# Kernel optimization log

Measured on AMD Instinct MI355X. Metric: run time of the kernel, lower is better.

## Reference

```python
import jax, jax.numpy as jnp
import numpy as np

D_MODEL = 256
D_HEAD = 64
N_HEAD = 8


def setup_inputs() -> dict:
    key = jax.random.key(0)
    ks = jax.random.split(key, 8)
    b, h, w = 32, 64, 64
    dk = D_HEAD * N_HEAD
    s = 1.0 / np.sqrt(D_MODEL)
    x = jax.random.normal(ks[0], (b, D_MODEL, h, w), dtype=jnp.float32)
    query = jax.random.normal(ks[1], (b, D_MODEL), dtype=jnp.float32)
    Wkv = jax.random.uniform(ks[2], (2 * dk, D_MODEL), jnp.float32, -s, s)
    bkv = jax.random.uniform(ks[3], (2 * dk,), jnp.float32, -s, s)
    Wq = jax.random.uniform(ks[4], (dk, D_MODEL), jnp.float32, -s, s)
    bq = jax.random.uniform(ks[5], (dk,), jnp.float32, -s, s)
    sf = 1.0 / np.sqrt(dk)
    Wfc = jax.random.uniform(ks[6], (D_MODEL, dk), jnp.float32, -sf, sf)
    bfc = jax.random.uniform(ks[7], (D_MODEL,), jnp.float32, -sf, sf)
    return {"x": x, "query": query, "Wkv": Wkv, "bkv": bkv, "Wq": Wq, "bq": bq, "Wfc": Wfc, "bfc": bfc}


def reference(x, query, Wkv, bkv, Wq, bq, Wfc, bfc):
    b, c, h, w = x.shape
    t = h * w
    scale = 1.0 / np.sqrt(D_HEAD).astype(np.float32)
    # 1x1 conv == per-pixel linear: (b, 2*n*d, t)
    kv = jnp.einsum('bchw,oc->bohw', x, Wkv).reshape(b, 2 * N_HEAD, D_HEAD, t)
    kv = kv + bkv.reshape(1, 2 * N_HEAD, D_HEAD, 1)
    k, v = kv[:, :N_HEAD], kv[:, N_HEAD:]  # each (b, n, d, t)
    q = (query @ Wq.T + bq).reshape(b, N_HEAD, D_HEAD)
    logits = jnp.einsum('bnd,bndj->bnj', q, k) * scale
    attn = jax.nn.softmax(logits, axis=2)
    out = jnp.einsum('bnj,bndj->bnd', attn, v).reshape(b, N_HEAD * D_HEAD)
    return jax.nn.relu(out @ Wfc.T + bfc)
```

## Files before the change

### kernel.cpp

```cpp
#include <hip/hip_runtime.h>
#include <hip/hip_bf16.h>

#define B_     32
#define C_     256
#define T_     4096
#define NH_    8
#define DH_    64

__global__ __launch_bounds__(256) void k_prep(
    const float* __restrict__ query, const float* __restrict__ Wkv,
    const float* __restrict__ bkv, const float* __restrict__ Wq,
    const float* __restrict__ bq, float* __restrict__ qWt,
    float* __restrict__ qb) {
  const int n = blockIdx.x;
  const int b = blockIdx.y;
  const int t = threadIdx.x;
  __shared__ float qrow_s[C_];
  __shared__ float psum[4 * 64];
  __shared__ float qsh[64];
  __shared__ float pb_s[64];

  qrow_s[t] = query[(size_t)b * C_ + t];
  __syncthreads();

  {
    const int d = t & 63, ch = t >> 6;
    const float* wrow = Wq + (size_t)(n * DH_ + d) * C_ + ch * 64;
    const float* qr = qrow_s + ch * 64;
    float s = 0.f;
    #pragma unroll
    for (int c = 0; c < 64; c += 4) {
      float4 w = *(const float4*)(wrow + c);
      s += w.x * qr[c] + w.y * qr[c + 1] + w.z * qr[c + 2] + w.w * qr[c + 3];
    }
    psum[ch * 64 + d] = s;
  }
  __syncthreads();
  if (t < 64)
    qsh[t] = bq[n * DH_ + t] + psum[t] + psum[64 + t] + psum[128 + t] + psum[192 + t];
  __syncthreads();

  const float scale = 0.125f;
  {
    const float* wk = Wkv + (size_t)(n * DH_) * C_ + t;
    float acc = 0.f;
    #pragma unroll 8
    for (int dd = 0; dd < DH_; ++dd) acc += qsh[dd] * wk[(size_t)dd * C_];
    qWt[((size_t)b * C_ + t) * NH_ + n] = acc * scale;
  }
  if (t < 64) pb_s[t] = qsh[t] * bkv[n * DH_ + t];
  __syncthreads();
  if (t == 0) {
    float s = 0.f;
    #pragma unroll 8
    for (int dd = 0; dd < 64; ++dd) s += pb_s[dd];
    qb[b * NH_ + n] = s * scale;
  }
}

__global__ __launch_bounds__(256) void k_logits(
    const float* __restrict__ x, const float* __restrict__ qWt,
    const float* __restrict__ qbv, float* __restrict__ lgpart) {
  const int half = blockIdx.y;
  const int b = blockIdx.z;
  const int t = threadIdx.x;
  const int j = blockIdx.x * 512 + t * 2;
  __shared__ float qws[128 * NH_];

  {
    const float4 v = *(const float4*)(qWt + (size_t)b * (C_ * NH_) + half * 1024 + t * 4);
    *(float4*)(qws + t * 4) = v;
  }
  __syncthreads();

  const float* xb = x + ((size_t)b * C_ + half * 128) * T_ + j;
  const float* qb = qbv + b * NH_;

  float acc0[NH_], acc1[NH_];
  #pragma unroll
  for (int n = 0; n < NH_; ++n) {
    const float init = half ? 0.f : qb[n];
    acc0[n] = init; acc1[n] = init;
  }

  for (int c0 = 0; c0 < 128; c0 += 8) {
    float2 xv[8];
    #pragma unroll
    for (int cc = 0; cc < 8; ++cc)
      xv[cc] = *(const float2*)(xb + (size_t)(c0 + cc) * T_);
    #pragma unroll
    for (int cc = 0; cc < 8; ++cc) {
      const float4 w0 = *(const float4*)(qws + (c0 + cc) * 8);
      const float4 w1 = *(const float4*)(qws + (c0 + cc) * 8 + 4);
      acc0[0] += w0.x * xv[cc].x; acc1[0] += w0.x * xv[cc].y;
      acc0[1] += w0.y * xv[cc].x; acc1[1] += w0.y * xv[cc].y;
      acc0[2] += w0.z * xv[cc].x; acc1[2] += w0.z * xv[cc].y;
      acc0[3] += w0.w * xv[cc].x; acc1[3] += w0.w * xv[cc].y;
      acc0[4] += w1.x * xv[cc].x; acc1[4] += w1.x * xv[cc].y;
      acc0[5] += w1.y * xv[cc].x; acc1[5] += w1.y * xv[cc].y;
      acc0[6] += w1.z * xv[cc].x; acc1[6] += w1.z * xv[cc].y;
      acc0[7] += w1.w * xv[cc].x; acc1[7] += w1.w * xv[cc].y;
    }
  }

  float* lg = lgpart + (((size_t)half * B_ + b) * NH_) * T_ + j;
  #pragma unroll
  for (int n = 0; n < NH_; ++n) {
    float2 o; o.x = acc0[n]; o.y = acc1[n];
    *(float2*)(lg + (size_t)n * T_) = o;
  }
}

__global__ __launch_bounds__(256) void k_softmax(
    const float* __restrict__ lgpart, float* __restrict__ attn) {
  const size_t row = blockIdx.x;
  const float* p0 = lgpart + row * T_;
  const float* p1 = lgpart + ((size_t)B_ * NH_ + row) * T_;
  float* pa = attn + row * T_;
  const int t = threadIdx.x;
  float4 v[4];
  #pragma unroll
  for (int i = 0; i < 4; ++i) {
    float4 a = *(const float4*)(p0 + t * 4 + i * 1024);
    float4 c = *(const float4*)(p1 + t * 4 + i * 1024);
    v[i].x = a.x + c.x; v[i].y = a.y + c.y; v[i].z = a.z + c.z; v[i].w = a.w + c.w;
  }

  float m = -3.4e38f;
  #pragma unroll
  for (int i = 0; i < 4; ++i)
    m = fmaxf(m, fmaxf(fmaxf(v[i].x, v[i].y), fmaxf(v[i].z, v[i].w)));
  #pragma unroll
  for (int o = 32; o >= 1; o >>= 1) m = fmaxf(m, __shfl_xor(m, o));
  __shared__ float sm[4];
  if ((t & 63) == 0) sm[t >> 6] = m;
  __syncthreads();
  m = fmaxf(fmaxf(sm[0], sm[1]), fmaxf(sm[2], sm[3]));

  float s = 0.f;
  #pragma unroll
  for (int i = 0; i < 4; ++i) {
    v[i].x = expf(v[i].x - m); v[i].y = expf(v[i].y - m);
    v[i].z = expf(v[i].z - m); v[i].w = expf(v[i].w - m);
    s += v[i].x + v[i].y + v[i].z + v[i].w;
  }
  #pragma unroll
  for (int o = 32; o >= 1; o >>= 1) s += __shfl_xor(s, o);
  __shared__ float ss[4];
  if ((t & 63) == 0) ss[t >> 6] = s;
  __syncthreads();
  s = ss[0] + ss[1] + ss[2] + ss[3];
  const float inv = 1.0f / s;

  #pragma unroll
  for (int i = 0; i < 4; ++i) {
    v[i].x *= inv; v[i].y *= inv; v[i].z *= inv; v[i].w *= inv;
    *(float4*)(pa + t * 4 + i * 1024) = v[i];
  }
}

#define BJ_  256
#define BJS_ 32
#define XPITCH_ 33
__global__ __launch_bounds__(256) void k_xattn(
    const float* __restrict__ x, const float* __restrict__ attn,
    float* __restrict__ part) {
  const int jt = blockIdx.x;
  const int b  = blockIdx.y;
  const int j0 = jt * BJ_;
  const int t  = threadIdx.x;
  __shared__ float xs[C_ * XPITCH_];

  const float* xb = x + (size_t)b * C_ * T_;
  const float* ab = attn + (size_t)b * NH_ * T_ + j0;

  float acc[NH_];
  #pragma unroll
  for (int n = 0; n < NH_; ++n) acc[n] = 0.f;

  const int cr = t >> 3;
  const int jc = (t & 7) * 4;

  for (int sIt = 0; sIt < BJ_ / BJS_; ++sIt) {
    const int js = sIt * BJS_;
    __syncthreads();
    #pragma unroll
    for (int p = 0; p < 8; ++p) {
      const int c = cr + p * 32;
      float4 vv = *(const float4*)(xb + (size_t)c * T_ + j0 + js + jc);
      float* dst = &xs[c * XPITCH_ + jc];
      dst[0] = vv.x; dst[1] = vv.y; dst[2] = vv.z; dst[3] = vv.w;
    }
    __syncthreads();
    const float* xr = &xs[t * XPITCH_];
    #pragma unroll 4
    for (int jj = 0; jj < BJS_; ++jj) {
      const float xv = xr[jj];
      const int j = js + jj;
      #pragma unroll
      for (int n = 0; n < NH_; ++n)
        acc[n] += ab[(size_t)n * T_ + j] * xv;
    }
  }

  float* pb = part + ((size_t)b * 16 + jt) * (NH_ * C_);
  #pragma unroll
  for (int n = 0; n < NH_; ++n) pb[n * C_ + t] = acc[n];
}

__global__ __launch_bounds__(512) void k_tail(
    const float* __restrict__ part, const float* __restrict__ Wkv,
    const float* __restrict__ bkv, const float* __restrict__ Wfc,
    const float* __restrict__ bfc, float* __restrict__ out) {
  __shared__ float xa_s[NH_ * C_];
  __shared__ float ov[512];
  const int b = blockIdx.x;
  const int t = threadIdx.x;

  const float* pb = part + (size_t)b * 16 * (NH_ * C_);
  #pragma unroll
  for (int r = 0; r < 4; ++r) {
    const int idx = r * 512 + t;
    float s = 0.f;
    #pragma unroll
    for (int jt = 0; jt < 16; ++jt) s += pb[(size_t)jt * (NH_ * C_) + idx];
    xa_s[idx] = s;
  }
  __syncthreads();

  {
    const int o = t;
    const float* wrow = Wkv + (size_t)(512 + o) * C_;
    const float* xa = &xa_s[(o >> 6) * C_];
    float s = bkv[512 + o];
    #pragma unroll 8
    for (int c = 0; c < C_; c += 4) {
      float4 w = *(const float4*)(wrow + c);
      s += w.x * xa[c] + w.y * xa[c + 1] + w.z * xa[c + 2] + w.w * xa[c + 3];
    }
    ov[o] = s;
  }
  __syncthreads();

  if (t < 256) {
    const int m = t;
    const float* wrow = Wfc + (size_t)m * 512;
    float s = bfc[m];
    #pragma unroll 8
    for (int o = 0; o < 512; o += 4) {
      float4 w = *(const float4*)(wrow + o);
      s += w.x * ov[o] + w.y * ov[o + 1] + w.z * ov[o + 2] + w.w * ov[o + 3];
    }
    out[(size_t)b * 256 + m] = fmaxf(s, 0.f);
  }
}

extern "C" void kernel_launch(void* const* d_in, const int* in_sizes, int n_in,
                              void* d_out, int out_size, void* d_ws, size_t ws_size,
                              hipStream_t stream) {
  const float* x     = (const float*)d_in[0];
  const float* query = (const float*)d_in[1];
  const float* Wkv   = (const float*)d_in[2];
  const float* bkv   = (const float*)d_in[3];
  const float* Wq    = (const float*)d_in[4];
  const float* bq    = (const float*)d_in[5];
  const float* Wfc   = (const float*)d_in[6];
  const float* bfc   = (const float*)d_in[7];
  float* out = (float*)d_out;
  float* ws  = (float*)d_ws;

  float* qWt    = ws;
  float* qb     = ws + 65536;
  float* lgpart = ws + 66048;
  float* attn   = ws + 2163200;
  float* part   = ws + 3211776;

  k_prep   <<<dim3(NH_, B_),   256, 0, stream>>>(query, Wkv, bkv, Wq, bq, qWt, qb);
  k_logits <<<dim3(8, 2, B_),  256, 0, stream>>>(x, qWt, qb, lgpart);
  k_softmax<<<B_ * NH_,        256, 0, stream>>>(lgpart, attn);
  k_xattn  <<<dim3(16, B_),    256, 0, stream>>>(x, attn, part);
  k_tail   <<<B_,              512, 0, stream>>>(part, Wkv, bkv, Wfc, bfc, out);
}
```

Baseline: 277.9 us.

## Fuse logits, softmax and attention-weighted x into one tiled split-softmax kernel

Replaces the separate logits, softmax and x·attn kernels with one kernel that loads each 64-column tile of x into shared memory once. It computes logits, local max and exponentials, and partial weighted sums per tile, then a merge kernel rescales the partials with the tile statistics (a flash-decoding-style split softmax). This removes the second full read of x and the global round trips for logits and attention weights. In exchange it writes larger partials (64 tiles per batch), serialises the per-tile softmax on 8 threads, and uses about 75KB of shared memory per block, which limits occupancy.

```diff
diff --git a/kernel.cpp b/kernel.cpp
--- a/kernel.cpp
+++ b/kernel.cpp
@@ -6,6 +6,9 @@
 #define T_     4096
 #define NH_    8
 #define DH_    64
+#define JT_    64
+#define NT_    (T_ / JT_)
+#define XP_    65
 
 __global__ __launch_bounds__(256) void k_prep(
     const float* __restrict__ query, const float* __restrict__ Wkv,
@@ -58,158 +61,137 @@
   }
 }
 
-__global__ __launch_bounds__(256) void k_logits(
+__global__ __launch_bounds__(256) void k_fused(
     const float* __restrict__ x, const float* __restrict__ qWt,
-    const float* __restrict__ qbv, float* __restrict__ lgpart) {
-  const int half = blockIdx.y;
-  const int b = blockIdx.z;
+    const float* __restrict__ qbv, float* __restrict__ part,
+    float* __restrict__ stats) {
+  const int tile = blockIdx.x;
+  const int b    = blockIdx.y;
+  const int t    = threadIdx.x;
+  const int j0   = tile * JT_;
+
+  __shared__ float xs[C_ * XP_];
+  __shared__ float lsc[4 * 576];
+  float* const ew = lsc + 576;
+
+  const float* xb = x + (size_t)b * C_ * T_ + j0;
+
+  {
+    const int cg = t >> 4;
+    const int jc = (t & 15) * 4;
+    #pragma unroll 4
+    for (int p = 0; p < 16; ++p) {
+      const int c = cg + p * 16;
+      float4 v = *(const float4*)(xb + (size_t)c * T_ + jc);
+      float* d = &xs[c * XP_ + jc];
+      d[0] = v.x; d[1] = v.y; d[2] = v.z; d[3] = v.w;
+    }
+  }
+  __syncthreads();
+
+  {
+    const int j  = t & 63;
+    const int ch = t >> 6;
+    const float* qw = qWt + ((size_t)b * C_ + ch * 64) * NH_;
+    float al[NH_];
+    #pragma unroll
+    for (int n = 0; n < NH_; ++n) al[n] = 0.f;
+    #pragma unroll 4
+    for (int cc = 0; cc < 64; ++cc) {
+      const float xv = xs[(ch * 64 + cc) * XP_ + j];
+      const float* qwc = qw + cc * NH_;
+      #pragma unroll
+      for (int n = 0; n < NH_; ++n) al[n] += qwc[n] * xv;
+    }
+    float* dst = &lsc[ch * 576 + j * 9];
+    #pragma unroll
+    for (int n = 0; n < NH_; ++n) dst[n] = al[n];
+  }
+  __syncthreads();
+
+  {
+    const float* qb = qbv + b * NH_;
+    #pragma unroll
+    for (int r = 0; r < 2; ++r) {
+      const int s = r * 256 + t;
+      const int j = s >> 3, n = s & 7;
+      const int idx = j * 9 + n;
+      const float l = lsc[idx] + lsc[576 + idx] + lsc[1152 + idx] +
+                      lsc[1728 + idx] + qb[n];
+      lsc[idx] = l;
+    }
+  }
+  __syncthreads();
+
+  if (t < NH_) {
+    float m = -3.4e38f;
+    for (int j = 0; j < JT_; ++j) m = fmaxf(m, lsc[j * 9 + t]);
+    float s = 0.f;
+    for (int j = 0; j < JT_; ++j) {
+      const float e = __expf(lsc[j * 9 + t] - m);
+      ew[j * 8 + t] = e;
+      s += e;
+    }
+    float* st = stats + (((size_t)b * NT_ + tile) * NH_ + t) * 2;
+    st[0] = m; st[1] = s;
+  }
+  __syncthreads();
+
+  {
+    float acc[NH_];
+    #pragma unroll
+    for (int n = 0; n < NH_; ++n) acc[n] = 0.f;
+    const float* xr = &xs[t * XP_];
+    #pragma unroll 4
+    for (int j = 0; j < JT_; ++j) {
+      const float xv = xr[j];
+      const float4 e0 = *(const float4*)(ew + j * 8);
+      const float4 e1 = *(const float4*)(ew + j * 8 + 4);
+      acc[0] += e0.x * xv; acc[1] += e0.y * xv;
+      acc[2] += e0.z * xv; acc[3] += e0.w * xv;
+      acc[4] += e1.x * xv; acc[5] += e1.y * xv;
+      acc[6] += e1.z * xv; acc[7] += e1.w * xv;
+    }
+    float* pb = part + (((size_t)b * NT_ + tile) * NH_) * C_;
+    #pragma unroll
+    for (int n = 0; n < NH_; ++n) pb[n * C_ + t] = acc[n];
+  }
+}
+
+__global__ __launch_bounds__(256) void k_merge(
+    const float* __restrict__ part, const float* __restrict__ stats,
+    float* __restrict__ xattnG) {
+  const int n = blockIdx.x;
+  const int b = blockIdx.y;
   const int t = threadIdx.x;
-  const int j = blockIdx.x * 512 + t * 2;
-  __shared__ float qws[128 * NH_];
-
-  {
-    const float4 v = *(const float4*)(qWt + (size_t)b * (C_ * NH_) + half * 1024 + t * 4);
-    *(float4*)(qws + t * 4) = v;
-  }
-  __syncthreads();
-
-  const float* xb = x + ((size_t)b * C_ + half * 128) * T_ + j;
-  const float* qb = qbv + b * NH_;
-
-  float acc0[NH_], acc1[NH_];
-  #pragma unroll
-  for (int n = 0; n < NH_; ++n) {
-    const float init = half ? 0.f : qb[n];
-    acc0[n] = init; acc1[n] = init;
-  }
-
-  for (int c0 = 0; c0 < 128; c0 += 8) {
-    float2 xv[8];
-    #pragma unroll
-    for (int cc = 0; cc < 8; ++cc)
-      xv[cc] = *(const float2*)(xb + (size_t)(c0 + cc) * T_);
-    #pragma unroll
-    for (int cc = 0; cc < 8; ++cc) {
-      const float4 w0 = *(const float4*)(qws + (c0 + cc) * 8);
-      const float4 w1 = *(const float4*)(qws + (c0 + cc) * 8 + 4);
-      acc0[0] += w0.x * xv[cc].x; acc1[0] += w0.x * xv[cc].y;
-      acc0[1] += w0.y * xv[cc].x; acc1[1] += w0.y * xv[cc].y;
-      acc0[2] += w0.z * xv[cc].x; acc1[2] += w0.z * xv[cc].y;
-      acc0[3] += w0.w * xv[cc].x; acc1[3] += w0.w * xv[cc].y;
-      acc0[4] += w1.x * xv[cc].x; acc1[4] += w1.x * xv[cc].y;
-      acc0[5] += w1.y * xv[cc].x; acc1[5] += w1.y * xv[cc].y;
-      acc0[6] += w1.z * xv[cc].x; acc1[6] += w1.z * xv[cc].y;
-      acc0[7] += w1.w * xv[cc].x; acc1[7] += w1.w * xv[cc].y;
-    }
-  }
-
-  float* lg = lgpart + (((size_t)half * B_ + b) * NH_) * T_ + j;
-  #pragma unroll
-  for (int n = 0; n < NH_; ++n) {
-    float2 o; o.x = acc0[n]; o.y = acc1[n];
-    *(float2*)(lg + (size_t)n * T_) = o;
-  }
-}
-
-__global__ __launch_bounds__(256) void k_softmax(
-    const float* __restrict__ lgpart, float* __restrict__ attn) {
-  const size_t row = blockIdx.x;
-  const float* p0 = lgpart + row * T_;
-  const float* p1 = lgpart + ((size_t)B_ * NH_ + row) * T_;
-  float* pa = attn + row * T_;
-  const int t = threadIdx.x;
-  float4 v[4];
-  #pragma unroll
-  for (int i = 0; i < 4; ++i) {
-    float4 a = *(const float4*)(p0 + t * 4 + i * 1024);
-    float4 c = *(const float4*)(p1 + t * 4 + i * 1024);
-    v[i].x = a.x + c.x; v[i].y = a.y + c.y; v[i].z = a.z + c.z; v[i].w = a.w + c.w;
-  }
-
-  float m = -3.4e38f;
-  #pragma unroll
-  for (int i = 0; i < 4; ++i)
-    m = fmaxf(m, fmaxf(fmaxf(v[i].x, v[i].y), fmaxf(v[i].z, v[i].w)));
-  #pragma unroll
-  for (int o = 32; o >= 1; o >>= 1) m = fmaxf(m, __shfl_xor(m, o));
-  __shared__ float sm[4];
-  if ((t & 63) == 0) sm[t >> 6] = m;
-  __syncthreads();
-  m = fmaxf(fmaxf(sm[0], sm[1]), fmaxf(sm[2], sm[3]));
-
-  float s = 0.f;
-  #pragma unroll
-  for (int i = 0; i < 4; ++i) {
-    v[i].x = expf(v[i].x - m); v[i].y = expf(v[i].y - m);
-    v[i].z = expf(v[i].z - m); v[i].w = expf(v[i].w - m);
-    s += v[i].x + v[i].y + v[i].z + v[i].w;
-  }
-  #pragma unroll
-  for (int o = 32; o >= 1; o >>= 1) s += __shfl_xor(s, o);
-  __shared__ float ss[4];
-  if ((t & 63) == 0) ss[t >> 6] = s;
-  __syncthreads();
-  s = ss[0] + ss[1] + ss[2] + ss[3];
-  const float inv = 1.0f / s;
-
-  #pragma unroll
-  for (int i = 0; i < 4; ++i) {
-    v[i].x *= inv; v[i].y *= inv; v[i].z *= inv; v[i].w *= inv;
-    *(float4*)(pa + t * 4 + i * 1024) = v[i];
-  }
-}
-
-#define BJ_  256
-#define BJS_ 32
-#define XPITCH_ 33
-__global__ __launch_bounds__(256) void k_xattn(
-    const float* __restrict__ x, const float* __restrict__ attn,
-    float* __restrict__ part) {
-  const int jt = blockIdx.x;
-  const int b  = blockIdx.y;
-  const int j0 = jt * BJ_;
-  const int t  = threadIdx.x;
-  __shared__ float xs[C_ * XPITCH_];
-
-  const float* xb = x + (size_t)b * C_ * T_;
-  const float* ab = attn + (size_t)b * NH_ * T_ + j0;
-
-  float acc[NH_];
-  #pragma unroll
-  for (int n = 0; n < NH_; ++n) acc[n] = 0.f;
-
-  const int cr = t >> 3;
-  const int jc = (t & 7) * 4;
-
-  for (int sIt = 0; sIt < BJ_ / BJS_; ++sIt) {
-    const int js = sIt * BJS_;
-    __syncthreads();
-    #pragma unroll
-    for (int p = 0; p < 8; ++p) {
-      const int c = cr + p * 32;
-      float4 vv = *(const float4*)(xb + (size_t)c * T_ + j0 + js + jc);
-      float* dst = &xs[c * XPITCH_ + jc];
-      dst[0] = vv.x; dst[1] = vv.y; dst[2] = vv.z; dst[3] = vv.w;
-    }
-    __syncthreads();
-    const float* xr = &xs[t * XPITCH_];
-    #pragma unroll 4
-    for (int jj = 0; jj < BJS_; ++jj) {
-      const float xv = xr[jj];
-      const int j = js + jj;
-      #pragma unroll
-      for (int n = 0; n < NH_; ++n)
-        acc[n] += ab[(size_t)n * T_ + j] * xv;
-    }
-  }
-
-  float* pb = part + ((size_t)b * 16 + jt) * (NH_ * C_);
-  #pragma unroll
-  for (int n = 0; n < NH_; ++n) pb[n * C_ + t] = acc[n];
+  __shared__ float mm[NT_], sv[NT_], wsc[NT_];
+
+  if (t < NT_) {
+    const float* st = stats + (((size_t)b * NT_ + t) * NH_ + n) * 2;
+    mm[t] = st[0]; sv[t] = st[1];
+  }
+  __syncthreads();
+
+  float M = -3.4e38f;
+  #pragma unroll 8
+  for (int i = 0; i < NT_; ++i) M = fmaxf(M, mm[i]);
+  if (t < NT_) wsc[t] = __expf(mm[t] - M);
+  __syncthreads();
+  float Z = 0.f;
+  #pragma unroll 8
+  for (int i = 0; i < NT_; ++i) Z += sv[i] * wsc[i];
+  const float invZ = 1.0f / Z;
+
+  const float* pb = part + (((size_t)b * NT_) * NH_ + n) * C_ + t;
+  float acc = 0.f;
+  #pragma unroll 4
+  for (int i = 0; i < NT_; ++i)
+    acc += wsc[i] * pb[(size_t)i * NH_ * C_];
+  xattnG[((size_t)b * NH_ + n) * C_ + t] = acc * invZ;
 }
 
 __global__ __launch_bounds__(512) void k_tail(
-    const float* __restrict__ part, const float* __restrict__ Wkv,
+    const float* __restrict__ xattnG, const float* __restrict__ Wkv,
     const float* __restrict__ bkv, const float* __restrict__ Wfc,
     const float* __restrict__ bfc, float* __restrict__ out) {
   __shared__ float xa_s[NH_ * C_];
@@ -217,15 +199,9 @@
   const int b = blockIdx.x;
   const int t = threadIdx.x;
 
-  const float* pb = part + (size_t)b * 16 * (NH_ * C_);
   #pragma unroll
-  for (int r = 0; r < 4; ++r) {
-    const int idx = r * 512 + t;
-    float s = 0.f;
-    #pragma unroll
-    for (int jt = 0; jt < 16; ++jt) s += pb[(size_t)jt * (NH_ * C_) + idx];
-    xa_s[idx] = s;
-  }
+  for (int r = 0; r < 4; ++r)
+    xa_s[r * 512 + t] = xattnG[(size_t)b * (NH_ * C_) + r * 512 + t];
   __syncthreads();
 
   {
@@ -271,13 +247,12 @@
 
   float* qWt    = ws;
   float* qb     = ws + 65536;
-  float* lgpart = ws + 66048;
-  float* attn   = ws + 2163200;
-  float* part   = ws + 3211776;
-
-  k_prep   <<<dim3(NH_, B_),   256, 0, stream>>>(query, Wkv, bkv, Wq, bq, qWt, qb);
-  k_logits <<<dim3(8, 2, B_),  256, 0, stream>>>(x, qWt, qb, lgpart);
-  k_softmax<<<B_ * NH_,        256, 0, stream>>>(lgpart, attn);
-  k_xattn  <<<dim3(16, B_),    256, 0, stream>>>(x, attn, part);
-  k_tail   <<<B_,              512, 0, stream>>>(part, Wkv, bkv, Wfc, bfc, out);
-}
+  float* part   = ws + 66048;
+  float* stats  = ws + 4260352;
+  float* xattnG = ws + 4293120;
+
+  k_prep <<<dim3(NH_, B_), 256, 0, stream>>>(query, Wkv, bkv, Wq, bq, qWt, qb);
+  k_fused<<<dim3(NT_, B_), 256, 0, stream>>>(x, qWt, qb, part, stats);
+  k_merge<<<dim3(NH_, B_), 256, 0, stream>>>(part, stats, xattnG);
+  k_tail <<<B_,            512, 0, stream>>>(xattnG, Wkv, bkv, Wfc, bfc, out);
+}
```

Result: slower. 296.1 us (+6.6%).
